# Optimization experiments

Hardware: AMD Instinct MI355X
Metric: run time of the kernel (lower is better)

Reference implementation:

```python
import jax, jax.numpy as jnp
import numpy as np

B, T, H, W, P = 2, 4, 224, 224, 16
D, DI, NS, RK, KC = 768, 1536, 16, 48, 4
DEPTH = 16
NV, NA = 196, 24                 # video/audio patches per frame
NTOT = (NV + 2 + NA + 2) * T     # 896 tokens (cls + patches + global, both modalities)
LVIS = NTOT // 2                 # 448 visible tokens


def setup_inputs():
    key = jax.random.key(0)
    ks = iter(jax.random.split(key, 64))
    def nrm(shape, s=0.02):
        return jax.random.normal(next(ks), shape, jnp.float32) * s
    inp = {}
    inp['x_v'] = jax.random.normal(next(ks), (B, 3, T, H, W), jnp.float32)
    inp['x_a'] = jax.random.normal(next(ks), (B, 64, 96 * T), jnp.float32)
    inp['patch_v_w'] = nrm((D, 3, P, P)); inp['patch_v_b'] = jnp.zeros((D,), jnp.float32)
    inp['patch_a_w'] = nrm((D, 1, P, P)); inp['patch_a_b'] = jnp.zeros((D,), jnp.float32)
    inp['pos_v'] = nrm((1, NV, D)); inp['pos_a'] = nrm((1, NA, D))
    inp['tpos_v'] = nrm((1, T, D)); inp['tpos_a'] = nrm((1, T, D))
    inp['cls_v'] = nrm((1, 1, D)); inp['cls_a'] = nrm((1, 1, D))
    inp['glob_v'] = nrm((1, 1, D)); inp['glob_a'] = nrm((1, 1, D))
    inp['norm_w'] = jnp.ones((DEPTH, D), jnp.float32)
    inp['in_w'] = nrm((DEPTH, 2 * DI, D))
    inp['conv_w'] = nrm((DEPTH, DI, KC), 0.2); inp['conv_b'] = jnp.zeros((DEPTH, DI), jnp.float32)
    inp['conv_w_b'] = nrm((DEPTH, DI, KC), 0.2); inp['conv_b_b'] = jnp.zeros((DEPTH, DI), jnp.float32)
    inp['xproj_w'] = nrm((DEPTH, RK + 2 * NS, DI))
    inp['xproj_w_b'] = nrm((DEPTH, RK + 2 * NS, DI))
    inp['dt_w'] = nrm((DEPTH, DI, RK), 0.1)
    inp['dt_w_b'] = nrm((DEPTH, DI, RK), 0.1)
    # mamba dt-bias init: inverse-softplus of dt ~ logU[1e-3, 0.1]
    lo, hi = np.log(1e-3), np.log(0.1)
    u = jax.random.uniform(next(ks), (DEPTH, DI), jnp.float32)
    dt = jnp.exp(u * (hi - lo) + lo)
    inp['dt_b'] = dt + jnp.log(-jnp.expm1(-dt))
    u2 = jax.random.uniform(next(ks), (DEPTH, DI), jnp.float32)
    dt2 = jnp.exp(u2 * (hi - lo) + lo)
    inp['dt_b_b'] = dt2 + jnp.log(-jnp.expm1(-dt2))
    alog = jnp.log(jnp.arange(1, NS + 1, dtype=jnp.float32))  # S4D-real init
    inp['A_log'] = jnp.broadcast_to(alog, (DEPTH, DI, NS)) + 0.0
    inp['A_log_b'] = jnp.broadcast_to(alog, (DEPTH, DI, NS)) + 0.0
    inp['D_par'] = jnp.ones((DEPTH, DI), jnp.float32)
    inp['D_par_b'] = jnp.ones((DEPTH, DI), jnp.float32)
    inp['out_w'] = nrm((DEPTH, D, DI))
    rng = np.random.default_rng(0)
    vi = np.stack([np.sort(rng.choice(NTOT, LVIS, replace=False)) for _ in range(B)])
    inp['vis_idx'] = jnp.asarray(vi, jnp.int32)
    return inp


def _causal_conv1d(x, w, b):
    # x: [B,L,DI]; depthwise causal conv, kernel KC
    xt = x.transpose(0, 2, 1)
    y = jax.lax.conv_general_dilated(xt, w[:, None, :], (1,), [(KC - 1, 0)], feature_group_count=DI)
    return (y + b[None, :, None]).transpose(0, 2, 1)


def _ssd(xc, dt, Bm, Cm, A, Dp):
    # selective scan: xc,dt [B,L,DI]; Bm,Cm [B,L,NS]; A [DI,NS]
    dA = jnp.exp(dt[..., None] * A)                         # B,L,DI,NS
    dBx = dt[..., None] * Bm[:, :, None, :] * xc[..., None]
    def step(h, s):
        a, bx, c = s
        h = a * h + bx
        return h, jnp.einsum('bdn,bn->bd', h, c)
    h0 = jnp.zeros((xc.shape[0], DI, NS), xc.dtype)
    _, ys = jax.lax.scan(step, h0, (jnp.swapaxes(dA, 0, 1), jnp.swapaxes(dBx, 0, 1), jnp.swapaxes(Cm, 0, 1)))
    return jnp.swapaxes(ys, 0, 1) + xc * Dp


def _mamba_dir(xi, zi, cw, cb, xw, dw, db, alog, dp):
    xc = jax.nn.silu(_causal_conv1d(xi, cw, cb))
    proj = jnp.einsum('bld,ed->ble', xc, xw)
    dtr, Bm, Cm = jnp.split(proj, [RK, RK + NS], axis=-1)
    dt = jax.nn.softplus(jnp.einsum('blr,dr->bld', dtr, dw) + db)
    y = _ssd(xc, dt, Bm, Cm, -jnp.exp(alog), dp)
    return y * jax.nn.silu(zi)


def reference(x_v, x_a, patch_v_w, patch_v_b, patch_a_w, patch_a_b, pos_v, pos_a, tpos_v, tpos_a,
              cls_v, cls_a, glob_v, glob_a, norm_w, in_w, conv_w, conv_b, conv_w_b, conv_b_b,
              xproj_w, xproj_w_b, dt_w, dt_b, dt_w_b, dt_b_b, A_log, A_log_b, D_par, D_par_b,
              out_w, vis_idx):
    Bn = x_v.shape[0]
    # video patch embed: conv3d k=(1,16,16) as unfold + matmul
    xv = x_v.transpose(0, 2, 3, 4, 1).reshape(Bn, T, H // P, P, W // P, P, 3)
    xv = xv.transpose(0, 1, 2, 4, 3, 5, 6).reshape(Bn, T, NV, P * P * 3)
    wv = patch_v_w.transpose(0, 2, 3, 1).reshape(D, -1)   # (kh,kw,c) flattening order
    xv = xv @ wv.T + patch_v_b                            # B,T,196,D
    # audio patch embed: [B,64,TA] -> [B,1,TA,64] conv2d 16x16
    TA = x_a.shape[-1]
    xa = x_a.transpose(0, 2, 1).reshape(Bn, TA // P, P, 64 // P, P)
    xa = xa.transpose(0, 1, 3, 2, 4).reshape(Bn, (TA // P) * (64 // P), P * P)
    xa = xa @ patch_a_w.reshape(D, -1).T + patch_a_b      # B, T*24, D
    xa = xa.reshape(Bn, T, NA, D)
    # spatial + temporal positional embeddings
    xv = xv + pos_v[None] + tpos_v[:, :, None, :]
    xa = xa + pos_a[None] + tpos_a[:, :, None, :]
    def add_tokens(x, cls, glob):
        BT = x.shape[0]
        return jnp.concatenate([jnp.broadcast_to(cls, (BT, 1, D)), x, jnp.broadcast_to(glob, (BT, 1, D))], 1)
    xv = add_tokens(xv.reshape(Bn * T, NV, D), cls_v, glob_v).reshape(Bn, T, NV + 2, D)
    xa = add_tokens(xa.reshape(Bn * T, NA, D), cls_a, glob_a).reshape(Bn, T, NA + 2, D)
    x = jnp.concatenate([xv, xa], 2).reshape(Bn, -1, D)   # B, 896, D
    x_vis = jnp.take_along_axis(x, vis_idx[:, :, None], axis=1)  # B, 448, D (x[~mask])

    def layer(carry, p):
        h, res = carry
        nw, iw, cw, cb, cwb, cbb, xw, xwb, dw, db, dwb, dbb, al, alb, dp, dpb, ow = p
        res = h + res                                     # fused add (drop_path=identity at eval)
        hn = res * jax.lax.rsqrt(jnp.mean(res * res, -1, keepdims=True) + 1e-5) * nw  # RMSNorm
        xz = jnp.einsum('bld,ed->ble', hn, iw)
        xi, zi = jnp.split(xz, 2, axis=-1)
        yf = _mamba_dir(xi, zi, cw, cb, xw, dw, db, al, dp)
        yb = _mamba_dir(xi[:, ::-1], zi[:, ::-1], cwb, cbb, xwb, dwb, dbb, alb, dpb)
        h = jnp.einsum('bld,ed->ble', yf + yb[:, ::-1], ow)
        return (h, res), None

    carry = (x_vis, jnp.zeros_like(x_vis))
    (h, res), _ = jax.lax.scan(layer, carry, (norm_w, in_w, conv_w, conv_b, conv_w_b, conv_b_b,
                                              xproj_w, xproj_w_b, dt_w, dt_b, dt_w_b, dt_b_b,
                                              A_log, A_log_b, D_par, D_par_b, out_w))
    # clip_return_layer=1 -> return_index=[depth-1]; only the post-loop append of the
    # final residual fires, so forward_features returns stack([residual]) of shape [1,B,L,D]
    return res[None]
```

## Files before the change

kernel.cpp:

```cpp
#include <hip/hip_runtime.h>
#include <math.h>

typedef unsigned short ushort_t;
typedef __attribute__((ext_vector_type(8))) short bf16x8;
typedef __attribute__((ext_vector_type(4))) float f32x4;
typedef __attribute__((ext_vector_type(4))) unsigned short us4;
typedef __attribute__((ext_vector_type(8))) unsigned short us8;

#define NBATCH 2
#define TT 4
#define DD 768
#define DI_ 1536
#define NS_ 16
#define RK_ 48
#define KC_ 4
#define DEPTH_ 16
#define NRUN 15
#define LV 448
#define NROWS (NBATCH*LV)
#define NCH 7
#define CLEN 64

#define WIN_SZ   (NRUN*2359296)
#define WOUT_SZ  (NRUN*1179648)
#define WX_SZ    (NRUN*2*196608)
#define WALL_USH (WIN_SZ + WOUT_SZ + WX_SZ)

__device__ __forceinline__ float silu_f(float x) { return x / (1.f + __expf(-x)); }
__device__ __forceinline__ ushort_t f2bf(float x) {
  unsigned int u = __float_as_uint(x);
  return (ushort_t)((u + 0x7FFFu + ((u >> 16) & 1u)) >> 16);
}
__device__ __forceinline__ float bf2f(ushort_t h) {
  return __uint_as_float(((unsigned int)h) << 16);
}

typedef const __attribute__((address_space(1))) unsigned int* gas1_t;
typedef __attribute__((address_space(3))) unsigned int* las3_t;
__device__ __forceinline__ void gll16(const ushort_t* g, ushort_t* l) {
  __builtin_amdgcn_global_load_lds((gas1_t)g, (las3_t)l, 16, 0, 0);
}

__global__ __launch_bounds__(256) void mfma_gemm(
    const ushort_t* __restrict__ A, const ushort_t* __restrict__ A2, int lda,
    const ushort_t* __restrict__ W, const ushort_t* __restrict__ W2, int ldw,
    const float* __restrict__ bias, const float* __restrict__ bias2,
    float* __restrict__ C, float* __restrict__ C2, int ldc,
    int M, int K, int nkChunks, long partStride, int epi)
{
  int z = blockIdx.z;
  int dir = z / nkChunks, chunk = z - dir * nkChunks;
  if (dir) { A = A2; W = W2; C = C2; bias = bias2; }
  int kChunk = K / nkChunks;
  int kbeg = chunk * kChunk;
  if (nkChunks > 1) C += (long)chunk * partStride;

  __shared__ __align__(16) ushort_t At[64 * 32];
  __shared__ __align__(16) ushort_t Bt[128 * 32];

  int tid = threadIdx.x, wv = tid >> 6, lane = tid & 63;
  int m0 = blockIdx.y * 64, n0 = blockIdx.x * 128;

  int rA = tid >> 2, gA = (tid & 3) ^ ((rA >> 1) & 3);
  const ushort_t* aSrc = A + (size_t)min(m0 + rA, M - 1) * lda + gA * 8 + kbeg;
  ushort_t* aDst = At + tid * 8;
  int SB0 = tid, SB1 = tid + 256;
  int rB0 = SB0 >> 2, gB0 = (SB0 & 3) ^ ((rB0 >> 1) & 3);
  int rB1 = SB1 >> 2, gB1 = (SB1 & 3) ^ ((rB1 >> 1) & 3);
  const ushort_t* bSrc0 = W + (size_t)(n0 + rB0) * ldw + gB0 * 8 + kbeg;
  const ushort_t* bSrc1 = W + (size_t)(n0 + rB1) * ldw + gB1 * 8 + kbeg;
  ushort_t* bDst0 = Bt + SB0 * 8;
  ushort_t* bDst1 = Bt + SB1 * 8;

  int wr = wv >> 1, wc = wv & 1;
  int rl = lane & 15, gl = lane >> 4;
  int offA[2], offB[4];
#pragma unroll
  for (int i = 0; i < 2; ++i) {
    int ra = wr * 32 + i * 16 + rl;
    offA[i] = ra * 32 + ((gl ^ ((ra >> 1) & 3)) * 8);
  }
#pragma unroll
  for (int j = 0; j < 4; ++j) {
    int rb = wc * 64 + j * 16 + rl;
    offB[j] = rb * 32 + ((gl ^ ((rb >> 1) & 3)) * 8);
  }

  f32x4 acc[2][4] = {};
  int nk = kChunk >> 5;
  for (int t = 0; t < nk; ++t) {
    int ko = t << 5;
    gll16(aSrc + ko, aDst);
    gll16(bSrc0 + ko, bDst0);
    gll16(bSrc1 + ko, bDst1);
    __syncthreads();
    bf16x8 af[2], bw[4];
#pragma unroll
    for (int i = 0; i < 2; ++i) af[i] = *(const bf16x8*)(At + offA[i]);
#pragma unroll
    for (int j = 0; j < 4; ++j) bw[j] = *(const bf16x8*)(Bt + offB[j]);
#pragma unroll
    for (int i = 0; i < 2; ++i)
#pragma unroll
      for (int j = 0; j < 4; ++j)
        acc[i][j] = __builtin_amdgcn_mfma_f32_16x16x32_bf16(af[i], bw[j], acc[i][j], 0, 0, 0);
    __syncthreads();
  }

#pragma unroll
  for (int i = 0; i < 2; ++i) {
    int row0 = m0 + wr * 32 + i * 16 + gl * 4;
#pragma unroll
    for (int q = 0; q < 4; ++q) {
      int row = row0 + q;
      if (row >= M) continue;
#pragma unroll
      for (int j = 0; j < 4; ++j) {
        int col = n0 + wc * 64 + j * 16 + rl;
        float v = acc[i][j][q];
        if (bias) v += bias[col];
        if (epi & 1) v = (v > 20.f) ? v : log1pf(__expf(v));
        if (epi & 2) ((ushort_t*)C)[(size_t)row * ldc + col] = f2bf(v);
        else C[(size_t)row * ldc + col] = v;
      }
    }
  }
}

__global__ __launch_bounds__(256) void cast4_k(const float* __restrict__ s, ushort_t* __restrict__ d, int n4)
{
  int i = blockIdx.x * 256 + threadIdx.x;
  if (i >= n4) return;
  f32x4 v = *(const f32x4*)(s + i * 4);
  us4 o = { f2bf(v[0]), f2bf(v[1]), f2bf(v[2]), f2bf(v[3]) };
  *(us4*)(d + i * 4) = o;
}

__global__ __launch_bounds__(256) void cast8_k(const float* __restrict__ s, ushort_t* __restrict__ d, int n8)
{
  int i = blockIdx.x * 256 + threadIdx.x;
  if (i >= n8) return;
  f32x4 v0 = *(const f32x4*)(s + i * 8);
  f32x4 v1 = *(const f32x4*)(s + i * 8 + 4);
  us8 o = { f2bf(v0[0]), f2bf(v0[1]), f2bf(v0[2]), f2bf(v0[3]),
            f2bf(v1[0]), f2bf(v1[1]), f2bf(v1[2]), f2bf(v1[3]) };
  *(us8*)(d + i * 8) = o;
}

__global__ __launch_bounds__(256) void castx8_k(
    const float* __restrict__ xw0, const float* __restrict__ xwb0,
    ushort_t* __restrict__ WX, int nl)
{
  int i = blockIdx.x * 256 + threadIdx.x;
  if (i >= nl * 2 * 24576) return;
  int ld = i / 24576;
  int j = (i - ld * 24576) * 8;
  int l = ld >> 1;
  const float* xs = ((ld & 1) ? xwb0 : xw0) + (size_t)l * 122880;
  int r = j / 1536, k = j - r * 1536;
  f32x4 v0 = {0.f,0.f,0.f,0.f}, v1 = {0.f,0.f,0.f,0.f};
  if (r < 80) { v0 = *(const f32x4*)(xs + r * 1536 + k); v1 = *(const f32x4*)(xs + r * 1536 + k + 4); }
  us8 o = { f2bf(v0[0]), f2bf(v0[1]), f2bf(v0[2]), f2bf(v0[3]),
            f2bf(v1[0]), f2bf(v1[1]), f2bf(v1[2]), f2bf(v1[3]) };
  *(us8*)(WX + (size_t)ld * 196608 + j) = o;
}

__global__ __launch_bounds__(256) void im2col_v(const float* __restrict__ xv, ushort_t* __restrict__ Av)
{
  int i = blockIdx.x * 256 + threadIdx.x;
  if (i >= 1568 * 768) return;
  int m = i / 768, k = i % 768;
  int c = k >> 8, r = k & 255;
  int kh = r >> 4, kw = r & 15;
  int bt = m / 196, n = m % 196;
  int b = bt / TT, t = bt % TT;
  int hb = n / 14, wb = n % 14;
  Av[i] = f2bf(xv[(size_t)b * 602112 + (size_t)c * 200704 + t * 50176 + (hb * 16 + kh) * 224 + wb * 16 + kw]);
}

__global__ __launch_bounds__(256) void im2col_a(const float* __restrict__ xa, ushort_t* __restrict__ Aa)
{
  int i = blockIdx.x * 256 + threadIdx.x;
  if (i >= 192 * 256) return;
  int m = i / 256, k = i % 256;
  int kh = k >> 4, kw = k & 15;
  int b = m / 96, q = m % 96;
  int tb = q >> 2, fb = q & 3;
  Aa[i] = f2bf(xa[(size_t)b * 24576 + (fb * 16 + kw) * 384 + tb * 16 + kh]);
}

__global__ __launch_bounds__(256) void assemble_k(
    const float* __restrict__ tokv, const float* __restrict__ toka,
    const float* __restrict__ pos_v, const float* __restrict__ pos_a,
    const float* __restrict__ tpos_v, const float* __restrict__ tpos_a,
    const float* __restrict__ cls_v, const float* __restrict__ cls_a,
    const float* __restrict__ glob_v, const float* __restrict__ glob_a,
    const int* __restrict__ vis_idx,
    float* __restrict__ h, float* __restrict__ res)
{
  int i = blockIdx.x * 256 + threadIdx.x;
  if (i >= NROWS * DD) return;
  int d = i % DD;
  int bl = i / DD;
  int r = bl % LV, b = bl / LV;
  int tok = vis_idx[b * LV + r];
  int t = tok / 224, q = tok % 224;
  float v;
  if (q == 0) v = cls_v[d];
  else if (q <= 196) {
    int n = q - 1;
    v = tokv[((size_t)(b * TT + t) * 196 + n) * DD + d] + pos_v[n * DD + d] + tpos_v[t * DD + d];
  } else if (q == 197) v = glob_v[d];
  else if (q == 198) v = cls_a[d];
  else if (q <= 222) {
    int n = q - 199;
    v = toka[((size_t)b * 96 + t * 24 + n) * DD + d] + pos_a[n * DD + d] + tpos_a[t * DD + d];
  } else v = glob_a[d];
  h[i] = v;
  res[i] = 0.f;
}

__global__ __launch_bounds__(256) void rmsnorm_k(
    const float* __restrict__ hsrc, const float* __restrict__ part,
    float* __restrict__ res, ushort_t* __restrict__ hn, const float* __restrict__ nw)
{
  int row = blockIdx.x;
  float* rp = res + (size_t)row * DD;
  ushort_t* op = hn + (size_t)row * DD;
  int tid = threadIdx.x;
  float v[3];
  float ss = 0.f;
#pragma unroll
  for (int i = 0; i < 3; ++i) {
    int c = tid + i * 256;
    float x;
    if (part) {
      x = part[(size_t)row * DD + c] + part[688128 + (size_t)row * DD + c]
        + part[2 * 688128 + (size_t)row * DD + c] + part[3 * 688128 + (size_t)row * DD + c];
    } else {
      x = hsrc[(size_t)row * DD + c];
    }
    x += rp[c];
    v[i] = x;
    ss += x * x;
  }
  for (int m = 1; m < 64; m <<= 1) ss += __shfl_xor(ss, m, 64);
  __shared__ float sred[4];
  if ((tid & 63) == 0) sred[tid >> 6] = ss;
  __syncthreads();
  float tot = sred[0] + sred[1] + sred[2] + sred[3];
  float sc = rsqrtf(tot / (float)DD + 1e-5f);
#pragma unroll
  for (int i = 0; i < 3; ++i) {
    int c = tid + i * 256;
    rp[c] = v[i];
    op[c] = f2bf(v[i] * sc * nw[c]);
  }
}

__global__ __launch_bounds__(256) void conv_k(
    const ushort_t* __restrict__ xz,
    const float* __restrict__ cw, const float* __restrict__ cb,
    const float* __restrict__ cwb, const float* __restrict__ cbb,
    ushort_t* __restrict__ xcFb, ushort_t* __restrict__ xcBb)
{
  int i = blockIdx.x * 256 + threadIdx.x;
  if (i >= NROWS * (DI_ / 4)) return;
  int dv = (i % (DI_ / 4)) * 4;
  int bl = i / (DI_ / 4);
  int l = bl % LV, b = bl / LV;
  const ushort_t* xzb = xz + (size_t)b * LV * (2 * DI_);
  f32x4 accf = *(const f32x4*)(cb + dv);
  f32x4 accb = *(const f32x4*)(cbb + dv);
  f32x4 tf[4], tb[4];
#pragma unroll
  for (int e = 0; e < 4; ++e) {
    tf[e] = *(const f32x4*)(cw + (dv + e) * 4);
    tb[e] = *(const f32x4*)(cwb + (dv + e) * 4);
  }
#pragma unroll
  for (int j = 0; j < 4; ++j) {
    int lp = l - 3 + j;
    if (lp >= 0) {
      us4 xf = *(const us4*)(xzb + (size_t)lp * (2 * DI_) + dv);
      us4 xb = *(const us4*)(xzb + (size_t)(LV - 1 - lp) * (2 * DI_) + dv);
#pragma unroll
      for (int e = 0; e < 4; ++e) {
        accf[e] += bf2f(xf[e]) * tf[e][j];
        accb[e] += bf2f(xb[e]) * tb[e][j];
      }
    }
  }
  us4 of, ob;
#pragma unroll
  for (int e = 0; e < 4; ++e) {
    of[e] = f2bf(silu_f(accf[e]));
    ob[e] = f2bf(silu_f(accb[e]));
  }
  *(us4*)(xcFb + (size_t)bl * DI_ + dv) = of;
  *(us4*)(xcBb + (size_t)bl * DI_ + dv) = ob;
}

__global__ __launch_bounds__(256) void reddt_k(
    const float* __restrict__ pF, const float* __restrict__ pB,
    float* __restrict__ prF, float* __restrict__ prB,
    const float* __restrict__ dwF, const float* __restrict__ dwB,
    const float* __restrict__ dbF, const float* __restrict__ dbB,
    ushort_t* __restrict__ dtFb, ushort_t* __restrict__ dtBb)
{
  int dir = blockIdx.y;
  const float* part = dir ? pB : pF;
  float* proj = dir ? prB : prF;
  const float* dw = dir ? dwB : dwF;
  const float* db = dir ? dbB : dbF;
  ushort_t* dt = dir ? dtBb : dtFb;
  int r0 = blockIdx.x * 8;
  int tid = threadIdx.x;
  __shared__ float sdtr[8][48];
  for (int o = tid; o < 8 * 80; o += 256) {
    int r = o / 80, col = o - (o / 80) * 80;
    int row = r0 + r;
    float s = 0.f;
#pragma unroll
    for (int c = 0; c < 8; ++c) s += part[c * (NROWS * 128) + row * 128 + col];
    proj[row * 80 + col] = s;
    if (col < 48) sdtr[r][col] = s;
  }
  __syncthreads();
#pragma unroll
  for (int q = 0; q < 6; ++q) {
    int d = q * 256 + tid;
    f32x4 w[12];
#pragma unroll
    for (int e = 0; e < 12; ++e) w[e] = *(const f32x4*)(dw + (size_t)d * 48 + e * 4);
    float bias = db[d];
#pragma unroll
    for (int r = 0; r < 8; ++r) {
      float s = bias;
#pragma unroll
      for (int e = 0; e < 12; ++e) {
#pragma unroll
        for (int u = 0; u < 4; ++u) s += sdtr[r][e * 4 + u] * w[e][u];
      }
      s = (s > 20.f) ? s : log1pf(__expf(s));
      dt[(size_t)(r0 + r) * DI_ + d] = f2bf(s);
    }
  }
}

__global__ __launch_bounds__(256) void scanA_k(
    const ushort_t* __restrict__ xcFb, const ushort_t* __restrict__ dtF, const float* __restrict__ prF,
    const ushort_t* __restrict__ xcBb, const ushort_t* __restrict__ dtB, const float* __restrict__ prB,
    const float* __restrict__ AlF, const float* __restrict__ AlB,
    float* __restrict__ hloc, float* __restrict__ Pb)
{
  int dir = blockIdx.z;
  const ushort_t* xc = dir ? xcBb : xcFb;
  const ushort_t* dt = dir ? dtB : dtF;
  const float* pr = dir ? prB : prF;
  const float* Al = dir ? AlB : AlF;
  int c = blockIdx.y;
  int g = blockIdx.x * 16 + (threadIdx.x >> 4);
  int n = threadIdx.x & 15;
  int b = g / DI_, d = g % DI_;
  float An = -__expf(Al[d * NS_ + n]);
  const ushort_t* xcp = xc + (size_t)b * LV * DI_ + d;
  const ushort_t* dtp = dt + (size_t)b * LV * DI_ + d;
  const float* prp = pr + (size_t)b * LV * 80;
  int l0 = c * CLEN;
  float hs = 0.f, S = 0.f;
  float dtv = bf2f(dtp[(size_t)l0 * DI_]);
  float xcv = bf2f(xcp[(size_t)l0 * DI_]);
  float bn  = prp[l0 * 80 + 48 + n];
  for (int kk = 0; kk < CLEN; ++kk) {
    float dtv_n = 0.f, xcv_n = 0.f, bn_n = 0.f;
    if (kk < CLEN - 1) {
      int l1 = l0 + kk + 1;
      dtv_n = bf2f(dtp[(size_t)l1 * DI_]);
      xcv_n = bf2f(xcp[(size_t)l1 * DI_]);
      bn_n  = prp[l1 * 80 + 48 + n];
    }
    hs = __expf(dtv * An) * hs + dtv * bn * xcv;
    S += dtv;
    dtv = dtv_n; xcv = xcv_n; bn = bn_n;
  }
  int idx = ((dir * 3072 + g) * 6 + c) * NS_ + n;
  hloc[idx] = hs;
  Pb[idx] = __expf(An * S);
}

__global__ __launch_bounds__(256) void scanBC_k(
    const ushort_t* __restrict__ xcFb, const ushort_t* __restrict__ dtF, const float* __restrict__ prF,
    const ushort_t* __restrict__ xcBb, const ushort_t* __restrict__ dtB, const float* __restrict__ prB,
    const float* __restrict__ AlF, const float* __restrict__ AlB,
    const float* __restrict__ DpF, const float* __restrict__ DpB,
    const float* __restrict__ hloc, const float* __restrict__ Pb,
    const ushort_t* __restrict__ xz, ushort_t* __restrict__ yc)
{
  int c = blockIdx.y;
  int tid = threadIdx.x;
  int n = tid & 15, gi = (tid >> 4) & 7, dir = tid >> 7;
  int g = blockIdx.x * 8 + gi;
  int b = g / DI_, d = g % DI_;
  __shared__ float sbuf[2][8][65];

  const ushort_t* xc = dir ? xcBb : xcFb;
  const ushort_t* dt = dir ? dtB : dtF;
  const float* pr = dir ? prB : prF;
  const float* Al = dir ? AlB : AlF;
  const float* Dpp = dir ? DpB : DpF;
  int myc = dir ? (6 - c) : c;
  float An = -__expf(Al[d * NS_ + n]);
  float Dpd = Dpp[d];
  float hs = 0.f;
  for (int j = 0; j < myc; ++j) {
    int idx = ((dir * 3072 + g) * 6 + j) * NS_ + n;
    hs = Pb[idx] * hs + hloc[idx];
  }
  const ushort_t* xcp = xc + (size_t)b * LV * DI_ + d;
  const ushort_t* dtp = dt + (size_t)b * LV * DI_ + d;
  const float* prp = pr + (size_t)b * LV * 80;
  int l0 = myc * CLEN;
  float dtv = bf2f(dtp[(size_t)l0 * DI_]);
  float xcv = bf2f(xcp[(size_t)l0 * DI_]);
  float bn  = prp[l0 * 80 + 48 + n];
  float cn  = prp[l0 * 80 + 64 + n];
  for (int kk = 0; kk < CLEN; ++kk) {
    float dtv_n = 0.f, xcv_n = 0.f, bn_n = 0.f, cn_n = 0.f;
    if (kk < CLEN - 1) {
      int l1 = l0 + kk + 1;
      dtv_n = bf2f(dtp[(size_t)l1 * DI_]);
      xcv_n = bf2f(xcp[(size_t)l1 * DI_]);
      bn_n  = prp[l1 * 80 + 48 + n];
      cn_n  = prp[l1 * 80 + 64 + n];
    }
    hs = __expf(dtv * An) * hs + dtv * bn * xcv;
    float p = hs * cn;
    p += __shfl_xor(p, 1, 16);
    p += __shfl_xor(p, 2, 16);
    p += __shfl_xor(p, 4, 16);
    p += __shfl_xor(p, 8, 16);
    if (n == 0) {
      int off = dir ? (CLEN - 1 - kk) : kk;
      sbuf[dir][gi][off] = p + xcv * Dpd;
    }
    dtv = dtv_n; xcv = xcv_n; bn = bn_n; cn = cn_n;
  }
  __syncthreads();
  for (int oid = tid; oid < 512; oid += 256) {
    int gi2 = oid & 7, kk = oid >> 3;
    int g2 = blockIdx.x * 8 + gi2;
    int b2 = g2 / DI_, d2 = g2 % DI_;
    int l = c * CLEN + kk;
    float z = bf2f(xz[((size_t)b2 * LV + l) * 3072 + 1536 + d2]);
    float v = (sbuf[0][gi2][kk] + sbuf[1][gi2][kk]) * silu_f(z);
    yc[((size_t)b2 * LV + l) * DI_ + d2] = f2bf(v);
  }
}

__global__ __launch_bounds__(256) void final_k(
    const float* __restrict__ res, const float* __restrict__ part, float* __restrict__ out)
{
  int i = blockIdx.x * 256 + threadIdx.x;
  if (i >= NROWS * DD) return;
  out[i] = res[i] + part[i] + part[688128 + i] + part[2 * 688128 + i] + part[3 * 688128 + i];
}

extern "C" void kernel_launch(void* const* d_in, const int* in_sizes, int n_in,
                              void* d_out, int out_size, void* d_ws, size_t ws_size,
                              hipStream_t stream)
{
  const float* x_v = (const float*)d_in[0];
  const float* x_a = (const float*)d_in[1];
  const float* patch_v_w = (const float*)d_in[2];
  const float* patch_v_b = (const float*)d_in[3];
  const float* patch_a_w = (const float*)d_in[4];
  const float* patch_a_b = (const float*)d_in[5];
  const float* pos_v = (const float*)d_in[6];
  const float* pos_a = (const float*)d_in[7];
  const float* tpos_v = (const float*)d_in[8];
  const float* tpos_a = (const float*)d_in[9];
  const float* cls_v = (const float*)d_in[10];
  const float* cls_a = (const float*)d_in[11];
  const float* glob_v = (const float*)d_in[12];
  const float* glob_a = (const float*)d_in[13];
  const float* norm_w = (const float*)d_in[14];
  const float* in_w = (const float*)d_in[15];
  const float* conv_w = (const float*)d_in[16];
  const float* conv_b = (const float*)d_in[17];
  const float* conv_w_b = (const float*)d_in[18];
  const float* conv_b_b = (const float*)d_in[19];
  const float* xproj_w = (const float*)d_in[20];
  const float* xproj_w_b = (const float*)d_in[21];
  const float *dt_w, *dt_bias, *dt_w_b, *dt_bias_b;
  if (in_sizes[23] == DEPTH_ * DI_ * RK_) {
    dt_w = (const float*)d_in[22]; dt_w_b = (const float*)d_in[23];
    dt_bias = (const float*)d_in[24]; dt_bias_b = (const float*)d_in[25];
  } else {
    dt_w = (const float*)d_in[22]; dt_bias = (const float*)d_in[23];
    dt_w_b = (const float*)d_in[24]; dt_bias_b = (const float*)d_in[25];
  }
  const float* A_log = (const float*)d_in[26];
  const float* A_log_b = (const float*)d_in[27];
  const float* D_par = (const float*)d_in[28];
  const float* D_par_b = (const float*)d_in[29];
  const float* out_w = (const float*)d_in[30];
  const int* vis_idx = (const int*)d_in[31];

  float* ws = (float*)d_ws;
  float* res   = ws;
  float* hbuf  = ws + 688128;
  float* R1    = ws + 1376256;
  float* R2f   = ws + 4128768;
  float* R3    = ws + 4816896;
  float* xz    = ws + 7569408;
  float* dtFf  = ws + 10321920;
  float* dtBf  = ws + 11698176;
  float* projF = ws + 13074432;
  float* projB = ws + 13146112;
  float* wPvf  = ws + 13217792;
  float* WALLf = ws + 13512704;

  float* partF = R1;
  float* partB = R1 + 917504;
  float* hloc  = R1;
  float* Pb    = R1 + 589824;
  float* partO = R1;
  float* tokv  = R1;
  float* toka  = R1 + 1204224;
  ushort_t* Av_bf = (ushort_t*)xz;
  ushort_t* wPv   = (ushort_t*)wPvf;
  ushort_t* wPa   = (ushort_t*)dtFf;
  ushort_t* Aa_bf = ((ushort_t*)dtFf) + 196608;
  ushort_t* hn_bf = (ushort_t*)R2f;
  ushort_t* ycb   = (ushort_t*)R2f;
  ushort_t* xcFb = (ushort_t*)R3;
  ushort_t* xcBb = ((ushort_t*)R3) + 1376256;
  ushort_t* xzb  = (ushort_t*)xz;
  ushort_t* dtFb = (ushort_t*)dtFf;
  ushort_t* dtBb = (ushort_t*)dtBf;

  size_t need_big = ((size_t)13512704 + (WALL_USH + 1) / 2) * 4;
  int bigws = ws_size >= need_big;
  ushort_t* WALL = (ushort_t*)WALLf;
  ushort_t* WIN  = WALL;
  ushort_t* WOUT = WIN + WIN_SZ;
  ushort_t* WX   = WOUT + WOUT_SZ;

  dim3 blk(256);

  if (bigws) {
    cast8_k<<<(WIN_SZ / 8 + 255) / 256, blk, 0, stream>>>(in_w, WIN, WIN_SZ / 8);
    cast8_k<<<(WOUT_SZ / 8 + 255) / 256, blk, 0, stream>>>(out_w, WOUT, WOUT_SZ / 8);
    castx8_k<<<(NRUN * 2 * 24576 + 255) / 256, blk, 0, stream>>>(xproj_w, xproj_w_b, WX, NRUN);
  }

  im2col_v<<<4704, blk, 0, stream>>>(x_v, Av_bf);
  cast4_k<<<576, blk, 0, stream>>>(patch_v_w, wPv, 147456);
  cast4_k<<<192, blk, 0, stream>>>(patch_a_w, wPa, 49152);
  im2col_a<<<192, blk, 0, stream>>>(x_a, Aa_bf);
  mfma_gemm<<<dim3(6, 25, 1), blk, 0, stream>>>(Av_bf, nullptr, 768, wPv, nullptr, 768,
                                                patch_v_b, nullptr, tokv, nullptr, 768,
                                                1568, 768, 1, 0, 0);
  mfma_gemm<<<dim3(6, 3, 1), blk, 0, stream>>>(Aa_bf, nullptr, 256, wPa, nullptr, 256,
                                               patch_a_b, nullptr, toka, nullptr, 768,
                                               192, 256, 1, 0, 0);
  assemble_k<<<2688, blk, 0, stream>>>(tokv, toka, pos_v, pos_a, tpos_v, tpos_a,
                                       cls_v, cls_a, glob_v, glob_a, vis_idx, hbuf, res);

  for (int l = 0; l < NRUN; ++l) {
    const float* nw  = norm_w + l * DD;
    const float* cw  = conv_w + l * DI_ * KC_;
    const float* cb  = conv_b + l * DI_;
    const float* cwb = conv_w_b + l * DI_ * KC_;
    const float* cbb = conv_b_b + l * DI_;
    const float* dwF = dt_w + (size_t)l * DI_ * RK_;
    const float* dwB = dt_w_b + (size_t)l * DI_ * RK_;
    const float* dbi = dt_bias + l * DI_;
    const float* dbib = dt_bias_b + l * DI_;
    const float* al  = A_log + (size_t)l * DI_ * NS_;
    const float* alb = A_log_b + (size_t)l * DI_ * NS_;
    const float* dp  = D_par + l * DI_;
    const float* dpb = D_par_b + l * DI_;

    ushort_t *wIn, *wOut, *wXF, *wXB;
    if (bigws) {
      wIn  = WIN + (size_t)l * 2359296;
      wOut = WOUT + (size_t)l * 1179648;
      wXF  = WX + (size_t)(l * 2) * 196608;
      wXB  = wXF + 196608;
    } else {
      wIn = WALL; wOut = wIn + 2359296; wXF = wOut + 1179648; wXB = wXF + 196608;
      cast8_k<<<(2359296 / 8 + 255) / 256, blk, 0, stream>>>(in_w + (size_t)l * 2359296, wIn, 2359296 / 8);
      cast8_k<<<(1179648 / 8 + 255) / 256, blk, 0, stream>>>(out_w + (size_t)l * 1179648, wOut, 1179648 / 8);
      castx8_k<<<(2 * 24576 + 255) / 256, blk, 0, stream>>>(xproj_w + (size_t)l * 122880,
                                                            xproj_w_b + (size_t)l * 122880, wXF, 1);
    }

    rmsnorm_k<<<NROWS, blk, 0, stream>>>(hbuf, l ? partO : nullptr, res, hn_bf, nw);
    mfma_gemm<<<dim3(24, 14, 1), blk, 0, stream>>>(hn_bf, nullptr, 768, wIn, nullptr, 768,
                                                   nullptr, nullptr, (float*)xzb, nullptr, 3072,
                                                   NROWS, 768, 1, 0, 2);
    conv_k<<<1344, blk, 0, stream>>>(xzb, cw, cb, cwb, cbb, xcFb, xcBb);
    mfma_gemm<<<dim3(1, 14, 16), blk, 0, stream>>>(xcFb, xcBb, 1536, wXF, wXB, 1536,
                                                   nullptr, nullptr, partF, partB, 128,
                                                   NROWS, 1536, 8, NROWS * 128, 0);
    reddt_k<<<dim3(112, 2, 1), blk, 0, stream>>>(partF, partB, projF, projB,
                                                 dwF, dwB, dbi, dbib, dtFb, dtBb);
    scanA_k<<<dim3(192, 6, 2), blk, 0, stream>>>(xcFb, dtFb, projF, xcBb, dtBb, projB,
                                                 al, alb, hloc, Pb);
    scanBC_k<<<dim3(384, NCH, 1), blk, 0, stream>>>(xcFb, dtFb, projF, xcBb, dtBb, projB,
                                                    al, alb, dp, dpb, hloc, Pb, xzb, ycb);
    mfma_gemm<<<dim3(6, 14, 4), blk, 0, stream>>>(ycb, nullptr, 1536, wOut, nullptr, 1536,
                                                  nullptr, nullptr, partO, nullptr, 768,
                                                  NROWS, 1536, 4, NROWS * DD, 0);
  }

  final_k<<<2688, blk, 0, stream>>>(res, partO, (float*)d_out);
}
```

Before: 2.567 ms.

## Triple-buffer LDS tiles in MFMA GEMM with async prefetch two steps ahead

The GEMM K-loop now uses three LDS buffers per operand and issues global_load_lds for tile t+2 while computing tile t. Explicit vmcnt waits replace the full __syncthreads drain, so up to two tiles of loads stay in flight and global latency overlaps the MFMA work. LDS use triples per block, which may lower occupancy, and correctness depends on the hand-written waitcnt counts matching the three loads issued per stage.

```diff
diff --git a/kernel.cpp b/kernel.cpp
--- a/kernel.cpp
+++ b/kernel.cpp
@@ -26,6 +26,9 @@
 #define WX_SZ    (NRUN*2*196608)
 #define WALL_USH (WIN_SZ + WOUT_SZ + WX_SZ)
 
+#define ABUF 2048
+#define BBUF 4096
+
 __device__ __forceinline__ float silu_f(float x) { return x / (1.f + __expf(-x)); }
 __device__ __forceinline__ ushort_t f2bf(float x) {
   unsigned int u = __float_as_uint(x);
@@ -55,22 +58,21 @@
   int kbeg = chunk * kChunk;
   if (nkChunks > 1) C += (long)chunk * partStride;
 
-  __shared__ __align__(16) ushort_t At[64 * 32];
-  __shared__ __align__(16) ushort_t Bt[128 * 32];
+  __shared__ __align__(16) ushort_t At[3 * ABUF];
+  __shared__ __align__(16) ushort_t Bt[3 * BBUF];
 
   int tid = threadIdx.x, wv = tid >> 6, lane = tid & 63;
   int m0 = blockIdx.y * 64, n0 = blockIdx.x * 128;
 
   int rA = tid >> 2, gA = (tid & 3) ^ ((rA >> 1) & 3);
   const ushort_t* aSrc = A + (size_t)min(m0 + rA, M - 1) * lda + gA * 8 + kbeg;
-  ushort_t* aDst = At + tid * 8;
+  int aOff = tid * 8;
   int SB0 = tid, SB1 = tid + 256;
   int rB0 = SB0 >> 2, gB0 = (SB0 & 3) ^ ((rB0 >> 1) & 3);
   int rB1 = SB1 >> 2, gB1 = (SB1 & 3) ^ ((rB1 >> 1) & 3);
   const ushort_t* bSrc0 = W + (size_t)(n0 + rB0) * ldw + gB0 * 8 + kbeg;
   const ushort_t* bSrc1 = W + (size_t)(n0 + rB1) * ldw + gB1 * 8 + kbeg;
-  ushort_t* bDst0 = Bt + SB0 * 8;
-  ushort_t* bDst1 = Bt + SB1 * 8;
+  int bOff0 = SB0 * 8, bOff1 = SB1 * 8;
 
   int wr = wv >> 1, wc = wv & 1;
   int rl = lane & 15, gl = lane >> 4;
@@ -88,23 +90,46 @@
 
   f32x4 acc[2][4] = {};
   int nk = kChunk >> 5;
+  gll16(aSrc, At + aOff);
+  gll16(bSrc0, Bt + bOff0);
+  gll16(bSrc1, Bt + bOff1);
+  if (nk > 1) {
+    gll16(aSrc + 32, At + ABUF + aOff);
+    gll16(bSrc0 + 32, Bt + BBUF + bOff0);
+    gll16(bSrc1 + 32, Bt + BBUF + bOff1);
+  }
+  int bufT = 0;
   for (int t = 0; t < nk; ++t) {
-    int ko = t << 5;
-    gll16(aSrc + ko, aDst);
-    gll16(bSrc0 + ko, bDst0);
-    gll16(bSrc1 + ko, bDst1);
-    __syncthreads();
+    int bufN = bufT + 2; if (bufN >= 3) bufN -= 3;
+    if (t + 2 < nk) {
+      int ko = (t + 2) << 5;
+      gll16(aSrc + ko, At + bufN * ABUF + aOff);
+      gll16(bSrc0 + ko, Bt + bufN * BBUF + bOff0);
+      gll16(bSrc1 + ko, Bt + bufN * BBUF + bOff1);
+      asm volatile("s_waitcnt vmcnt(6)" ::: "memory");
+    } else if (t + 1 < nk) {
+      asm volatile("s_waitcnt vmcnt(3)" ::: "memory");
+    } else {
+      asm volatile("s_waitcnt vmcnt(0)" ::: "memory");
+    }
+    __builtin_amdgcn_s_barrier();
+    __builtin_amdgcn_sched_barrier(0);
+    const ushort_t* Ab = At + bufT * ABUF;
+    const ushort_t* Bb = Bt + bufT * BBUF;
     bf16x8 af[2], bw[4];
 #pragma unroll
-    for (int i = 0; i < 2; ++i) af[i] = *(const bf16x8*)(At + offA[i]);
-#pragma unroll
-    for (int j = 0; j < 4; ++j) bw[j] = *(const bf16x8*)(Bt + offB[j]);
+    for (int i = 0; i < 2; ++i) af[i] = *(const bf16x8*)(Ab + offA[i]);
+#pragma unroll
+    for (int j = 0; j < 4; ++j) bw[j] = *(const bf16x8*)(Bb + offB[j]);
 #pragma unroll
     for (int i = 0; i < 2; ++i)
 #pragma unroll
       for (int j = 0; j < 4; ++j)
         acc[i][j] = __builtin_amdgcn_mfma_f32_16x16x32_bf16(af[i], bw[j], acc[i][j], 0, 0, 0);
-    __syncthreads();
+    asm volatile("s_waitcnt lgkmcnt(0)" ::: "memory");
+    __builtin_amdgcn_s_barrier();
+    __builtin_amdgcn_sched_barrier(0);
+    bufT += 1; if (bufT == 3) bufT = 0;
   }
 
 #pragma unroll
```

Result: no change. 2.544 ms (-0.9%).
